# Optimization experiments

Hardware: AMD Instinct MI355X
Metric: run time of the kernel (lower is better)

Reference implementation:

```python
import itertools
import jax, jax.numpy as jnp
import numpy as np

N_QUBITS = 32  # 2 * I, I = 16
LIST_GATES = [(2 * i, 2 * i + 1) for i in range(15)]


def _build_gate_mats(n, gates):
    """For each RBS gate (a,b) build the three structural matrices over the
    Hamming-weight-2 basis: cos-part (diag on single-occupancy states),
    sin-part (antisymmetric swap a<->b), identity-part (unaffected states).
    U(theta) = cos(theta)*Mc + sin(theta)*Ms + Mi.
    """
    pairs = list(itertools.combinations(range(n), 2))
    idx = {p: k for k, p in enumerate(pairs)}
    dim = len(pairs)
    G = len(gates)
    MC = np.zeros((G, dim, dim), np.float32)
    MS = np.zeros((G, dim, dim), np.float32)
    MI = np.zeros((G, dim, dim), np.float32)
    for g, (a, b) in enumerate(gates):
        for p, k in idx.items():
            has_a, has_b = (a in p), (b in p)
            if has_a != has_b:
                MC[g, k, k] = 1.0
                if has_a:  # partner state: a replaced by b
                    other = p[0] if p[1] == a else p[1]
                    kp = idx[tuple(sorted((other, b)))]
                    MS[g, k, kp] = 1.0
                    MS[g, kp, k] = -1.0
            else:  # both or neither qubit occupied -> identity action
                MI[g, k, k] = 1.0
    return jnp.asarray(MC), jnp.asarray(MS), jnp.asarray(MI)


_MC, _MS, _MI = _build_gate_mats(N_QUBITS, LIST_GATES)


def setup_inputs() -> dict:
    key = jax.random.key(0)
    k1, k2 = jax.random.split(key)
    dim = _MC.shape[1]  # 496 = C(32, 2)
    input_state = jax.random.normal(k1, (8, dim, dim), dtype=jnp.float32)
    angles = jax.random.uniform(k2, (len(LIST_GATES),), dtype=jnp.float32)
    return {"input_state": input_state, "angles": angles}


def reference(input_state, angles):
    # Sequentially apply each RBS gate: rho <- U rho U^T (real unitaries).
    def step(rho, gate):
        theta, mc, ms, mi = gate
        U = jnp.cos(theta) * mc + jnp.sin(theta) * ms + mi  # (dim, dim)
        rho = jnp.einsum('ij,bjk,lk->bil', U, rho, U)
        return rho, None

    out, _ = jax.lax.scan(step, input_state.astype(jnp.float32),
                          (angles, _MC, _MS, _MI))
    return out
```

## Files before the change

### kernel.cpp

```cpp
#include <hip/hip_runtime.h>

#define DIM 496

__device__ __forceinline__ int pair_idx(int r, int s) {
    return (r * (63 - r)) / 2 + (s - r - 1);
}

__device__ __forceinline__ void decode_pair(int i, int& p, int& q) {
    p = (int)((63.0f - sqrtf(3969.0f - 8.0f * (float)i)) * 0.5f);
    while ((p + 1) * (62 - p) / 2 <= i) ++p;
    while (p * (63 - p) / 2 > i) --p;
    q = i - p * (63 - p) / 2 + p + 1;
}

__device__ __forceinline__ void decode_gate_pair(int o, int& gp, int& gq) {
    gp = 0;
    while ((gp + 1) * (30 - gp) / 2 <= o) ++gp;
    gq = o - gp * (31 - gp) / 2 + gp + 1;
}

__global__ __launch_bounds__(256)
void rbs_orbit_kernel(const float* __restrict__ rho,
                      const float* __restrict__ ang,
                      float* __restrict__ out)
{
    __shared__ float sc[16], ss[16];
    __shared__ float v[4][DIM];

    const int tid = threadIdx.x;
    const int blk = blockIdx.x;
    const int b   = blockIdx.y;

    if (tid < 16) {
        float t = (tid < 15) ? ang[tid] : 0.0f;
        sc[tid] = cosf(t);
        ss[tid] = (tid < 15) ? sinf(t) : 0.0f;
    }
    __syncthreads();

    int rows[4];
    float M[4][4];
    if (blk < 120) {
        int gp, gq;
        decode_gate_pair(blk, gp, gq);
        const int p0 = 2 * gp, q0 = 2 * gq;
        rows[0] = pair_idx(p0,     q0);
        rows[1] = pair_idx(p0,     q0 + 1);
        rows[2] = pair_idx(p0 + 1, q0);
        rows[3] = pair_idx(p0 + 1, q0 + 1);
        const float cp = sc[gp], sp = ss[gp];
        const float cq = sc[gq], sq = ss[gq];
        const float up[2][2] = {{cp, sp}, {-sp, cp}};
        const float uq[2][2] = {{cq, sq}, {-sq, cq}};
        #pragma unroll
        for (int a = 0; a < 2; ++a)
            #pragma unroll
            for (int bb = 0; bb < 2; ++bb)
                #pragma unroll
                for (int c = 0; c < 2; ++c)
                    #pragma unroll
                    for (int d = 0; d < 2; ++d)
                        M[a * 2 + bb][c * 2 + d] = up[a][c] * uq[bb][d];
    } else {
        const int k = blk - 120;
        #pragma unroll
        for (int t = 0; t < 4; ++t) {
            const int g = 4 * k + t;
            rows[t] = pair_idx(2 * g, 2 * g + 1);
        }
        #pragma unroll
        for (int a = 0; a < 4; ++a)
            #pragma unroll
            for (int c = 0; c < 4; ++c)
                M[a][c] = (a == c) ? 1.0f : 0.0f;
    }

    const float* base = rho + (size_t)b * DIM * DIM;

    if (tid < 124) {
        const float4 x0 = reinterpret_cast<const float4*>(base + (size_t)rows[0] * DIM)[tid];
        const float4 x1 = reinterpret_cast<const float4*>(base + (size_t)rows[1] * DIM)[tid];
        const float4 x2 = reinterpret_cast<const float4*>(base + (size_t)rows[2] * DIM)[tid];
        const float4 x3 = reinterpret_cast<const float4*>(base + (size_t)rows[3] * DIM)[tid];
        #pragma unroll
        for (int r = 0; r < 4; ++r) {
            float4 y;
            y.x = M[r][0] * x0.x + M[r][1] * x1.x + M[r][2] * x2.x + M[r][3] * x3.x;
            y.y = M[r][0] * x0.y + M[r][1] * x1.y + M[r][2] * x2.y + M[r][3] * x3.y;
            y.z = M[r][0] * x0.z + M[r][1] * x1.z + M[r][2] * x2.z + M[r][3] * x3.z;
            y.w = M[r][0] * x0.w + M[r][1] * x1.w + M[r][2] * x2.w + M[r][3] * x3.w;
            reinterpret_cast<float4*>(&v[r][0])[tid] = y;
        }
    }
    __syncthreads();

    float* obase = out + (size_t)b * DIM * DIM;
    for (int j = tid; j < DIM; j += 256) {
        int pj, qj;
        decode_pair(j, pj, qj);
        float r0, r1, r2, r3;
        if ((pj >> 1) == (qj >> 1)) {
            r0 = v[0][j]; r1 = v[1][j]; r2 = v[2][j]; r3 = v[3][j];
        } else {
            const float wpp = sc[pj >> 1];
            const float wpP = (pj & 1) ? -ss[pj >> 1] : ss[pj >> 1];
            const float wqq = sc[qj >> 1];
            const float wqQ = (qj & 1) ? -ss[qj >> 1] : ss[qj >> 1];
            const int m1 = pair_idx(pj ^ 1, qj);
            const int m2 = pair_idx(pj, qj ^ 1);
            const int m3 = pair_idx(pj ^ 1, qj ^ 1);
            const float c0 = wpp * wqq, c1 = wpP * wqq;
            const float c2 = wpp * wqQ, c3 = wpP * wqQ;
            r0 = c0 * v[0][j] + c1 * v[0][m1] + c2 * v[0][m2] + c3 * v[0][m3];
            r1 = c0 * v[1][j] + c1 * v[1][m1] + c2 * v[1][m2] + c3 * v[1][m3];
            r2 = c0 * v[2][j] + c1 * v[2][m1] + c2 * v[2][m2] + c3 * v[2][m3];
            r3 = c0 * v[3][j] + c1 * v[3][m1] + c2 * v[3][m2] + c3 * v[3][m3];
        }
        obase[(size_t)rows[0] * DIM + j] = r0;
        obase[(size_t)rows[1] * DIM + j] = r1;
        obase[(size_t)rows[2] * DIM + j] = r2;
        obase[(size_t)rows[3] * DIM + j] = r3;
    }
}

extern "C" void kernel_launch(void* const* d_in, const int* in_sizes, int n_in,
                              void* d_out, int out_size, void* d_ws, size_t ws_size,
                              hipStream_t stream) {
    const float* rho = (const float*)d_in[0];
    const float* ang = (const float*)d_in[1];
    float* out = (float*)d_out;
    dim3 grid(124, 8, 1);
    rbs_orbit_kernel<<<grid, dim3(256, 1, 1), 0, stream>>>(rho, ang, out);
}
```

Baseline: 10.27 us.

## Issue row loads before trig setup and replace pair decode with shared lookup table

```diff
diff --git a/kernel.cpp b/kernel.cpp
--- a/kernel.cpp
+++ b/kernel.cpp
@@ -2,22 +2,8 @@
 
 #define DIM 496
 
-__device__ __forceinline__ int pair_idx(int r, int s) {
-    return (r * (63 - r)) / 2 + (s - r - 1);
-}
-
-__device__ __forceinline__ void decode_pair(int i, int& p, int& q) {
-    p = (int)((63.0f - sqrtf(3969.0f - 8.0f * (float)i)) * 0.5f);
-    while ((p + 1) * (62 - p) / 2 <= i) ++p;
-    while (p * (63 - p) / 2 > i) --p;
-    q = i - p * (63 - p) / 2 + p + 1;
-}
-
-__device__ __forceinline__ void decode_gate_pair(int o, int& gp, int& gq) {
-    gp = 0;
-    while ((gp + 1) * (30 - gp) / 2 <= o) ++gp;
-    gq = o - gp * (31 - gp) / 2 + gp + 1;
-}
+__device__ __forceinline__ int pair_off(int p) { return (p * (63 - p)) >> 1; }
+__device__ __forceinline__ int pair_idx(int r, int s) { return pair_off(r) + (s - r - 1); }
 
 __global__ __launch_bounds__(256)
 void rbs_orbit_kernel(const float* __restrict__ rho,
@@ -25,33 +11,67 @@
                       float* __restrict__ out)
 {
     __shared__ float sc[16], ss[16];
+    __shared__ unsigned char pp[DIM];
     __shared__ float v[4][DIM];
 
     const int tid = threadIdx.x;
     const int blk = blockIdx.x;
     const int b   = blockIdx.y;
 
-    if (tid < 16) {
-        float t = (tid < 15) ? ang[tid] : 0.0f;
-        sc[tid] = cosf(t);
-        ss[tid] = (tid < 15) ? sinf(t) : 0.0f;
-    }
-    __syncthreads();
-
     int rows[4];
-    float M[4][4];
+    int gp = 16, gq = 16;
     if (blk < 120) {
-        int gp, gq;
-        decode_gate_pair(blk, gp, gq);
+        gp = 0;
+        while ((gp + 1) * (30 - gp) / 2 <= blk) ++gp;
+        gq = blk - gp * (31 - gp) / 2 + gp + 1;
         const int p0 = 2 * gp, q0 = 2 * gq;
         rows[0] = pair_idx(p0,     q0);
         rows[1] = pair_idx(p0,     q0 + 1);
         rows[2] = pair_idx(p0 + 1, q0);
         rows[3] = pair_idx(p0 + 1, q0 + 1);
-        const float cp = sc[gp], sp = ss[gp];
-        const float cq = sc[gq], sq = ss[gq];
-        const float up[2][2] = {{cp, sp}, {-sp, cp}};
-        const float uq[2][2] = {{cq, sq}, {-sq, cq}};
+    } else {
+        const int k = blk - 120;
+        #pragma unroll
+        for (int t = 0; t < 4; ++t) {
+            const int g = 4 * k + t;
+            rows[t] = pair_idx(2 * g, 2 * g + 1);
+        }
+    }
+
+    const float* base = rho + (size_t)b * DIM * DIM;
+    const bool ld = (tid < 248);
+    float2 x0, x1, x2, x3;
+    if (ld) {
+        x0 = reinterpret_cast<const float2*>(base + (size_t)rows[0] * DIM)[tid];
+        x1 = reinterpret_cast<const float2*>(base + (size_t)rows[1] * DIM)[tid];
+        x2 = reinterpret_cast<const float2*>(base + (size_t)rows[2] * DIM)[tid];
+        x3 = reinterpret_cast<const float2*>(base + (size_t)rows[3] * DIM)[tid];
+    }
+
+    if (tid < 16) {
+        const float t = (tid < 15) ? ang[tid] : 0.0f;
+        float s, c;
+        __sincosf(t, &s, &c);
+        sc[tid] = c;
+        ss[tid] = (tid < 15) ? s : 0.0f;
+    }
+    if (tid >= 64 && tid < 126) {
+        const int l = tid - 64;
+        const int p = l >> 1;
+        const int off = pair_off(p);
+        for (int q = p + 1 + (l & 1); q < 32; q += 2)
+            pp[off + q - p - 1] = (unsigned char)p;
+    }
+
+    float M[4][4];
+    if (blk < 120) {
+        const float tp = ang[gp];
+        const float tq = (gq < 15) ? ang[gq] : 0.0f;
+        float sp_, cp, sq_, cq;
+        __sincosf(tp, &sp_, &cp);
+        __sincosf(tq, &sq_, &cq);
+        const float up[2][2] = {{cp, sp_}, {-sp_, cp}};
+        const float uq[2][2] = {{cq, sq_}, {-sq_, cq}};
         #pragma unroll
         for (int a = 0; a < 2; ++a)
             #pragma unroll
@@ -62,12 +82,6 @@
                     for (int d = 0; d < 2; ++d)
                         M[a * 2 + bb][c * 2 + d] = up[a][c] * uq[bb][d];
     } else {
-        const int k = blk - 120;
-        #pragma unroll
-        for (int t = 0; t < 4; ++t) {
-            const int g = 4 * k + t;
-            rows[t] = pair_idx(2 * g, 2 * g + 1);
-        }
         #pragma unroll
         for (int a = 0; a < 4; ++a)
             #pragma unroll
@@ -75,51 +89,49 @@
                 M[a][c] = (a == c) ? 1.0f : 0.0f;
     }
 
-    const float* base = rho + (size_t)b * DIM * DIM;
-
-    if (tid < 124) {
-        const float4 x0 = reinterpret_cast<const float4*>(base + (size_t)rows[0] * DIM)[tid];
-        const float4 x1 = reinterpret_cast<const float4*>(base + (size_t)rows[1] * DIM)[tid];
-        const float4 x2 = reinterpret_cast<const float4*>(base + (size_t)rows[2] * DIM)[tid];
-        const float4 x3 = reinterpret_cast<const float4*>(base + (size_t)rows[3] * DIM)[tid];
+    if (ld) {
         #pragma unroll
         for (int r = 0; r < 4; ++r) {
-            float4 y;
+            float2 y;
             y.x = M[r][0] * x0.x + M[r][1] * x1.x + M[r][2] * x2.x + M[r][3] * x3.x;
             y.y = M[r][0] * x0.y + M[r][1] * x1.y + M[r][2] * x2.y + M[r][3] * x3.y;
-            y.z = M[r][0] * x0.z + M[r][1] * x1.z + M[r][2] * x2.z + M[r][3] * x3.z;
-            y.w = M[r][0] * x0.w + M[r][1] * x1.w + M[r][2] * x2.w + M[r][3] * x3.w;
-            reinterpret_cast<float4*>(&v[r][0])[tid] = y;
+            reinterpret_cast<float2*>(&v[r][0])[tid] = y;
         }
     }
     __syncthreads();
 
     float* obase = out + (size_t)b * DIM * DIM;
-    for (int j = tid; j < DIM; j += 256) {
-        int pj, qj;
-        decode_pair(j, pj, qj);
-        float r0, r1, r2, r3;
-        if ((pj >> 1) == (qj >> 1)) {
-            r0 = v[0][j]; r1 = v[1][j]; r2 = v[2][j]; r3 = v[3][j];
-        } else {
-            const float wpp = sc[pj >> 1];
-            const float wpP = (pj & 1) ? -ss[pj >> 1] : ss[pj >> 1];
-            const float wqq = sc[qj >> 1];
-            const float wqQ = (qj & 1) ? -ss[qj >> 1] : ss[qj >> 1];
-            const int m1 = pair_idx(pj ^ 1, qj);
-            const int m2 = pair_idx(pj, qj ^ 1);
-            const int m3 = pair_idx(pj ^ 1, qj ^ 1);
-            const float c0 = wpp * wqq, c1 = wpP * wqq;
-            const float c2 = wpp * wqQ, c3 = wpP * wqQ;
-            r0 = c0 * v[0][j] + c1 * v[0][m1] + c2 * v[0][m2] + c3 * v[0][m3];
-            r1 = c0 * v[1][j] + c1 * v[1][m1] + c2 * v[1][m2] + c3 * v[1][m3];
-            r2 = c0 * v[2][j] + c1 * v[2][m1] + c2 * v[2][m2] + c3 * v[2][m3];
-            r3 = c0 * v[3][j] + c1 * v[3][m1] + c2 * v[3][m2] + c3 * v[3][m3];
+    #pragma unroll
+    for (int it = 0; it < 2; ++it) {
+        const int j = tid + it * 256;
+        if (j < DIM) {
+            const int p = pp[j];
+            const int q = j - pair_off(p) + p + 1;
+            const int g1 = p >> 1, g2 = q >> 1;
+            const bool id = (g1 == g2);
+            const int p1 = p ^ 1, q1 = q ^ 1;
+            const int m1 = id ? j : pair_idx(p1, q);
+            const int m2 = id ? j : pair_idx(p, q1);
+            const int m3 = id ? j : pair_idx(p1, q1);
+
+            const float cp = sc[g1], sp_ = ss[g1];
+            const float cq = sc[g2], sq_ = ss[g2];
+            const float upp = cp;
+            const float upP = (p & 1) ? -sp_ : sp_;
+            const float uqq = cq;
+            const float uqQ = (q & 1) ? -sq_ : sq_;
+            const float c0 = id ? 1.0f : upp * uqq;
+            const float c1 = id ? 0.0f : upP * uqq;
+            const float c2 = id ? 0.0f : upp * uqQ;
+            const float c3 = id ? 0.0f : upP * uqQ;
+
+            #pragma unroll
+            for (int r = 0; r < 4; ++r) {
+                const float res = c0 * v[r][j] + c1 * v[r][m1]
+                                + c2 * v[r][m2] + c3 * v[r][m3];
+                obase[(size_t)rows[r] * DIM + j] = res;
+            }
         }
-        obase[(size_t)rows[0] * DIM + j] = r0;
-        obase[(size_t)rows[1] * DIM + j] = r1;
-        obase[(size_t)rows[2] * DIM + j] = r2;
-        obase[(size_t)rows[3] * DIM + j] = r3;
     }
 }
 
```

Result: no change. 10.21 us (-0.6%).
